# Kernel optimization log

Measured on AMD Instinct MI355X. Metric: run time of the kernel, lower is better.

The kernel has to match this reference:

```python
import jax, jax.numpy as jnp
import numpy as np

EPS = 1e-12

def _safe_norm(x, axis):
    return jnp.sqrt(jnp.sum(x * x, axis=axis) + EPS)

def _forward(z, pos, edge_index, batch, batch_size, emb, centers, gamma,
             fw1, fb1, fw2, fb2, uw1, ub1, uw2, ub2,
             ew1, eb1, ew2, eb2, dipole_w, nac_w,
             aw1, ab1, aw2, ab2, yw1, yb1, yw2, yb2):
    row, col = edge_index[0], edge_index[1]
    N = pos.shape[0]
    diff = pos[col] - pos[row]                    # (E,3)
    dist = _safe_norm(diff, axis=1)               # (E,)
    dirs = diff / (dist[:, None] + 1e-8)          # (E,3)
    rbf = jnp.exp(-gamma * (dist[:, None] - centers) ** 2)   # (E,R)
    s = emb[z]                                    # (N,F)
    v = jnp.zeros((N, s.shape[1], 3), s.dtype)    # (N,F,3)
    n_layers = fw1.shape[0]
    for l in range(n_layers):
        # filter MLP on RBF features -> 3 gates per edge
        phi = jax.nn.silu(rbf @ fw1[l] + fb1[l]) @ fw2[l] + fb2[l]   # (E,3F)
        phi_ss, phi_vv, phi_sv = jnp.split(phi, 3, axis=-1)
        sc = s[col]                                                    # gather (E,F)
        m_s = jax.ops.segment_sum(phi_ss * sc, row, num_segments=N)    # (N,F)
        m_v_e = (phi_vv[..., None] * v[col]
                 + phi_sv[..., None] * dirs[:, None, :] * sc[..., None])  # (E,F,3)
        m_v = jax.ops.segment_sum(m_v_e, row, num_segments=N)          # (N,F,3)
        v_norm = _safe_norm(m_v, axis=-1)                              # (N,F)
        upd = (jax.nn.silu(jnp.concatenate([s, m_s, v_norm], axis=-1) @ uw1[l] + ub1[l])
               @ uw2[l] + ub2[l])                                       # (N,3F)
        delta_s, alpha, beta = jnp.split(upd, 3, axis=-1)
        s = s + delta_s
        v = alpha[..., None] * v + beta[..., None] * m_v
    # energy heads (stacked over states S)
    h = jax.nn.silu(jnp.einsum('nf,sfg->nsg', s, ew1) + eb1)           # (N,S,F)
    e_atom = (jnp.einsum('nsg,sgo->nso', h, ew2) + eb2)[..., 0]        # (N,S)
    energies = jax.ops.segment_sum(e_atom, batch, num_segments=batch_size)  # (M,S)
    dipoles = jax.ops.segment_sum(jnp.einsum('nfk,f->nk', v, dipole_w), batch,
                                  num_segments=batch_size)             # (M,3)
    nac = jax.ops.segment_sum(jnp.einsum('nfk,pf->npk', v, nac_w), batch,
                              num_segments=batch_size)                 # (M,P,3)
    gaps = energies[:, 1:] - energies[:, :1]                           # (M,S-1)
    lam = jax.nn.silu(gaps @ aw1 + ab1) @ aw2 + ab2                    # (M,1)
    nac_mag = _safe_norm(nac, axis=-1)                                 # (M,P)
    phi_y = jax.nn.sigmoid(
        jax.nn.silu(jnp.concatenate([gaps, nac_mag], axis=1) @ yw1 + yb1) @ yw2 + yb2)  # (M,1)
    return energies, dipoles, nac, lam, phi_y

N, E, F, R, L, S, M, A = 20000, 320000, 128, 20, 3, 4, 1000, 100
P = S - 1

def setup_inputs() -> dict:
    key = jax.random.key(0)
    ks = jax.random.split(key, 32)
    w = lambda i, shape, sc=0.05: jax.random.normal(ks[i], shape, jnp.float32) * sc
    return {
        'z': jax.random.randint(ks[0], (N,), 0, A),
        'pos': jax.random.normal(ks[1], (N, 3), jnp.float32),
        'edge_index': jax.random.randint(ks[2], (2, E), 0, N),
        'batch': jnp.sort(jax.random.randint(ks[3], (N,), 0, M)),
        'batch_size': M,
        'emb': jax.random.normal(ks[4], (A, F), jnp.float32),
        'centers': jnp.linspace(0.0, 5.0, R),
        'gamma': jnp.ones((R,), jnp.float32),
        'fw1': w(5, (L, R, F)), 'fb1': jnp.zeros((L, F)),
        'fw2': w(6, (L, F, 3 * F)), 'fb2': jnp.zeros((L, 3 * F)),
        'uw1': w(7, (L, 3 * F, F)), 'ub1': jnp.zeros((L, F)),
        'uw2': w(8, (L, F, 3 * F)), 'ub2': jnp.zeros((L, 3 * F)),
        'ew1': w(9, (S, F, F)), 'eb1': jnp.zeros((S, F)),
        'ew2': w(10, (S, F, 1)), 'eb2': jnp.zeros((S, 1)),
        'dipole_w': jax.random.normal(ks[11], (F,), jnp.float32),
        'nac_w': jax.random.normal(ks[12], (P, F), jnp.float32),
        'aw1': w(13, (S - 1, 64)), 'ab1': jnp.zeros((64,)),
        'aw2': w(14, (64, 1)), 'ab2': jnp.zeros((1,)),
        'yw1': w(15, (S - 1 + P, 128)), 'yb1': jnp.zeros((128,)),
        'yw2': w(16, (128, 1)), 'yb2': jnp.zeros((1,)),
    }

def reference(z, pos, edge_index, batch, batch_size, emb, centers, gamma,
              fw1, fb1, fw2, fb2, uw1, ub1, uw2, ub2,
              ew1, eb1, ew2, eb2, dipole_w, nac_w,
              aw1, ab1, aw2, ab2, yw1, yb1, yw2, yb2):
    return _forward(z, pos, edge_index, batch, batch_size, emb, centers, gamma,
                    fw1, fb1, fw2, fb2, uw1, ub1, uw2, ub2,
                    ew1, eb1, ew2, eb2, dipole_w, nac_w,
                    aw1, ab1, aw2, ab2, yw1, yb1, yw2, yb2)
```

## Files before the change

### kernel.cpp

```cpp
#include <hip/hip_runtime.h>
#include <hip/hip_fp16.h>

#define FDIM 128
#define RDIM 20

#define TAB_T 2048
#define TAB_RANGE 12.0f

constexpr int TH = 256;

__device__ __forceinline__ float siluf(float x) { return x / (1.f + __expf(-x)); }

__device__ __forceinline__ void store_h4(__half* p, float a, float b, float c, float d) {
    __half h[4] = {__float2half(a), __float2half(b), __float2half(c), __float2half(d)};
    *(uint2*)p = *(uint2*)h;
}

typedef _Float16 h2v __attribute__((ext_vector_type(2)));
__device__ __forceinline__ float fdot2u(unsigned int a, unsigned int b, float c) {
    union { unsigned int u; h2v h; } ua, ub;
    ua.u = a; ub.u = b;
    return __builtin_amdgcn_fdot2(ua.h, ub.h, c, false);
}

__global__ void k_init(const int* __restrict__ z, const float* __restrict__ emb,
                       float* __restrict__ s, __half* __restrict__ s_h, int N) {
    int i = blockIdx.x * blockDim.x + threadIdx.x;
    if (i >= N * FDIM) return;
    int n = i >> 7, f = i & 127;
    float val = emb[z[n] * FDIM + f];
    s[i] = val;
    s_h[i] = __float2half(val);
}

__global__ void k_packl(const float* __restrict__ src, unsigned int* __restrict__ dst,
                        int C, int total, size_t sstride, size_t dstride) {
    int l = blockIdx.y;
    const float* sp = src + (size_t)l * sstride;
    unsigned int* dp = dst + (size_t)l * dstride;
    int i = blockIdx.x * 256 + threadIdx.x;
    if (i >= total) return;
    int kp = i / C, c = i - kp * C;
    __half2 h = __halves2half2(__float2half(sp[(2*kp) * C + c]),
                               __float2half(sp[(2*kp+1) * C + c]));
    dp[i] = *(unsigned int*)&h;
}

__global__ void k_hist(const int* __restrict__ erow, int* __restrict__ cursor, int E) {
    int e = blockIdx.x * blockDim.x + threadIdx.x;
    if (e < E) atomicAdd(&cursor[erow[e]], 1);
}

__global__ __launch_bounds__(256) void k_scan1(const int* __restrict__ cursor,
                                               int* __restrict__ rowstart,
                                               int* __restrict__ bsum, int N) {
    __shared__ int sh[256];
    int tid = threadIdx.x;
    int idx = blockIdx.x * 256 + tid;
    int x = (idx < N) ? cursor[idx] : 0;
    sh[tid] = x;
    __syncthreads();
    #pragma unroll
    for (int off = 1; off < 256; off <<= 1) {
        int t = (tid >= off) ? sh[tid - off] : 0;
        __syncthreads();
        sh[tid] += t;
        __syncthreads();
    }
    if (idx < N) rowstart[idx] = sh[tid] - x;
    if (tid == 255) bsum[blockIdx.x] = sh[255];
}

__global__ __launch_bounds__(256) void k_scan2(int* __restrict__ bsum,
                                               int* __restrict__ rowstart, int nb, int N) {
    __shared__ int sh[256];
    __shared__ int carry;
    int tid = threadIdx.x;
    if (tid == 0) carry = 0;
    __syncthreads();
    for (int base = 0; base < nb; base += 256) {
        int idx = base + tid;
        int x = (idx < nb) ? bsum[idx] : 0;
        sh[tid] = x;
        __syncthreads();
        #pragma unroll
        for (int off = 1; off < 256; off <<= 1) {
            int t = (tid >= off) ? sh[tid - off] : 0;
            __syncthreads();
            sh[tid] += t;
            __syncthreads();
        }
        if (idx < nb) bsum[idx] = carry + sh[tid] - x;
        __syncthreads();
        if (tid == 0) carry += sh[255];
        __syncthreads();
    }
    if (tid == 0) rowstart[N] = carry;
}

__global__ __launch_bounds__(256) void k_scan3(int* __restrict__ rowstart,
                                               int* __restrict__ cursor,
                                               const int* __restrict__ bsum, int N) {
    int idx = blockIdx.x * 256 + threadIdx.x;
    if (idx < N) {
        int val = rowstart[idx] + bsum[blockIdx.x];
        rowstart[idx] = val;
        cursor[idx] = val;
    }
}

__global__ void k_fill(const int* __restrict__ erow, int* __restrict__ cursor,
                       int* __restrict__ esort, int E) {
    int e = blockIdx.x * blockDim.x + threadIdx.x;
    if (e < E) {
        int p = atomicAdd(&cursor[erow[e]], 1);
        esort[p] = e;
    }
}

__global__ void k_geom(const float* __restrict__ pos, const int* __restrict__ erow,
                       const int* __restrict__ ecol, const int* __restrict__ esort,
                       int2* __restrict__ geo_ci, float4* __restrict__ geo_wd,
                       float inv_step, int E) {
    int i = blockIdx.x * blockDim.x + threadIdx.x;
    if (i >= E) return;
    int e  = esort[i];
    int rw = erow[e], cl = ecol[e];
    float dx = pos[cl*3+0] - pos[rw*3+0];
    float dy = pos[cl*3+1] - pos[rw*3+1];
    float dz = pos[cl*3+2] - pos[rw*3+2];
    float dist = sqrtf(dx*dx + dy*dy + dz*dz + 1e-12f);
    float inv = 1.f / (dist + 1e-8f);
    float u = fminf(dist * inv_step, (float)TAB_T);
    int t0 = min((int)u, TAB_T - 1);
    geo_ci[i] = make_int2(cl, t0);
    geo_wd[i] = make_float4(u - (float)t0, dx*inv, dy*inv, dz*inv);
}

__global__ __launch_bounds__(TH) void k_table(
    const float* __restrict__ centers, const float* __restrict__ gamma,
    const float* __restrict__ fw1b, const float* __restrict__ fb1b,
    const float* __restrict__ fw2b, const float* __restrict__ fb2b,
    __half* __restrict__ tabb, float step)
{
    __shared__ float sh_rbf[32][RDIM];
    __shared__ float sh_ht[FDIM][33];
    __shared__ float sh_w[32][3 * FDIM + 4];

    const int l   = blockIdx.y;
    const float* fw1 = fw1b + (size_t)l * RDIM * FDIM;
    const float* fb1 = fb1b + (size_t)l * FDIM;
    const float* fw2 = fw2b + (size_t)l * FDIM * 3 * FDIM;
    const float* fb2 = fb2b + (size_t)l * 3 * FDIM;
    __half* tab = tabb + (size_t)l * (TAB_T + 1) * 384;

    const int p0  = blockIdx.x * 32;
    const int tid = threadIdx.x;

    for (int i = tid; i < 32 * RDIM; i += TH) {
        int p = i / RDIM, r = i - p * RDIM;
        float d = (float)(p0 + p) * step - centers[r];
        sh_rbf[p][r] = __expf(-gamma[r] * d * d);
    }
    __syncthreads();
    for (int i = tid; i < 32 * FDIM; i += TH) {
        int p = i >> 7, f = i & 127;
        float acc = fb1[f];
        #pragma unroll
        for (int r = 0; r < RDIM; ++r) acc += sh_rbf[p][r] * fw1[r * FDIM + f];
        sh_ht[f][p] = siluf(acc);
    }

    const int eq = tid & 7;
    const int fq = tid >> 3;
    const int f0 = fq * 4;

    float pg[3][4][4];
    #pragma unroll
    for (int g3 = 0; g3 < 3; ++g3)
        #pragma unroll
        for (int ee = 0; ee < 4; ++ee)
            #pragma unroll
            for (int i = 0; i < 4; ++i) pg[g3][ee][i] = fb2[g3 * FDIM + f0 + i];

    const int kkr = tid >> 3;
    const int t8  = tid & 7;
    for (int kc = 0; kc < 4; ++kc) {
        __syncthreads();
        #pragma unroll
        for (int j = 0; j < 12; ++j) {
            int g = (t8 * 12 + j) * 4;
            float4 w4 = *(const float4*)&fw2[(size_t)(kc * 32 + kkr) * (3 * FDIM) + g];
            *(float4*)&sh_w[kkr][g] = w4;
        }
        __syncthreads();
        #pragma unroll 4
        for (int kk = 0; kk < 32; ++kk) {
            float hv[4];
            #pragma unroll
            for (int ee = 0; ee < 4; ++ee) hv[ee] = sh_ht[kc * 32 + kk][4 * eq + ee];
            #pragma unroll
            for (int g3 = 0; g3 < 3; ++g3) {
                float4 w4 = *(const float4*)&sh_w[kk][g3 * FDIM + f0];
                #pragma unroll
                for (int ee = 0; ee < 4; ++ee) {
                    pg[g3][ee][0] += hv[ee] * w4.x;
                    pg[g3][ee][1] += hv[ee] * w4.y;
                    pg[g3][ee][2] += hv[ee] * w4.z;
                    pg[g3][ee][3] += hv[ee] * w4.w;
                }
            }
        }
    }

    #pragma unroll
    for (int ee = 0; ee < 4; ++ee) {
        int pt = p0 + 4 * eq + ee;
        if (pt <= TAB_T) {
            #pragma unroll
            for (int g3 = 0; g3 < 3; ++g3)
                store_h4(&tab[(size_t)pt * 384 + g3 * FDIM + f0],
                         pg[g3][ee][0], pg[g3][ee][1], pg[g3][ee][2], pg[g3][ee][3]);
        }
    }
}

__global__ __launch_bounds__(256) void k_repack(const __half* __restrict__ tab,
                                                __half2* __restrict__ tab2) {
    int l = blockIdx.y;
    const __half* t  = tab  + (size_t)l * (TAB_T + 1) * 384;
    __half2*      t2 = tab2 + (size_t)l * TAB_T * 384;
    int i = blockIdx.x * 256 + threadIdx.x;
    t2[i] = __halves2half2(t[i], t[i + 384]);
}

__global__ __launch_bounds__(128) void k_gather(
    const int* __restrict__ rowstart,
    const int2* __restrict__ geo_ci, const float4* __restrict__ geo_wd,
    const __half2* __restrict__ tab2, const __half* __restrict__ s_h,
    const __half* __restrict__ v_h,
    __half* __restrict__ m_s_h, __half* __restrict__ vnorm_h, __half* __restrict__ m_v_h,
    int withv, int N)
{
    __shared__ int   sh_col[32];
    __shared__ int   sh_t0[32];
    __shared__ float sh_w[32];
    __shared__ float sh_d0[32], sh_d1[32], sh_d2[32];

    const int n   = blockIdx.x;
    const int tid = threadIdx.x;
    const int lo  = rowstart[n], hi = rowstart[n + 1];

    float acc_s = 0.f, av0 = 0.f, av1 = 0.f, av2 = 0.f;

    for (int base = lo; base < hi; base += 32) {
        const int ne = min(32, hi - base);
        __syncthreads();
        if (tid < 32) {
            int idx = base + tid;
            if (tid < ne) {
                int2   ci = geo_ci[idx];
                float4 wd = geo_wd[idx];
                sh_col[tid] = ci.x; sh_t0[tid] = ci.y;
                sh_w[tid] = wd.x;
                sh_d0[tid] = wd.y; sh_d1[tid] = wd.z; sh_d2[tid] = wd.w;
            } else {
                sh_col[tid] = 0; sh_t0[tid] = 0; sh_w[tid] = 0.f;
                sh_d0[tid] = sh_d1[tid] = sh_d2[tid] = 0.f;
            }
        }
        __syncthreads();
        if (withv) {
            #pragma unroll 2
            for (int el = 0; el < ne; ++el) {
                int   cl = sh_col[el];
                int   t0 = sh_t0[el];
                float w  = sh_w[el];
                const __half2* t2 = tab2 + (size_t)t0 * 384 + tid;
                float2 pss2 = __half22float2(t2[0]);
                float2 pvv2 = __half22float2(t2[128]);
                float2 psv2 = __half22float2(t2[256]);
                float pss = pss2.x + w * (pss2.y - pss2.x);
                float pvv = pvv2.x + w * (pvv2.y - pvv2.x);
                float psv = psv2.x + w * (psv2.y - psv2.x);
                float sc = __half2float(s_h[(size_t)cl * FDIM + tid]);
                const __half* vp = v_h + (size_t)cl * 3 * FDIM + tid;
                float svs = psv * sc;
                acc_s += pss * sc;
                av0 += pvv * __half2float(vp[0])        + svs * sh_d0[el];
                av1 += pvv * __half2float(vp[FDIM])     + svs * sh_d1[el];
                av2 += pvv * __half2float(vp[2*FDIM])   + svs * sh_d2[el];
            }
        } else {
            #pragma unroll 2
            for (int el = 0; el < ne; ++el) {
                int   cl = sh_col[el];
                int   t0 = sh_t0[el];
                float w  = sh_w[el];
                const __half2* t2 = tab2 + (size_t)t0 * 384 + tid;
                float2 pss2 = __half22float2(t2[0]);
                float2 psv2 = __half22float2(t2[256]);
                float pss = pss2.x + w * (pss2.y - pss2.x);
                float psv = psv2.x + w * (psv2.y - psv2.x);
                float sc = __half2float(s_h[(size_t)cl * FDIM + tid]);
                float svs = psv * sc;
                acc_s += pss * sc;
                av0 += svs * sh_d0[el];
                av1 += svs * sh_d1[el];
                av2 += svs * sh_d2[el];
            }
        }
    }

    m_s_h[(size_t)n * FDIM + tid]  = __float2half(acc_s);
    vnorm_h[(size_t)n * FDIM + tid] = __float2half(sqrtf(av0*av0 + av1*av1 + av2*av2 + 1e-12f));
    __half* mh = m_v_h + (size_t)n * 3 * FDIM + tid;
    mh[0]      = __float2half(av0);
    mh[FDIM]   = __float2half(av1);
    mh[2*FDIM] = __float2half(av2);
}

__global__ __launch_bounds__(128) void k_mlp1(
    const __half* __restrict__ s_h, const __half* __restrict__ m_s_h,
    const __half* __restrict__ vnorm_h,
    const unsigned int* __restrict__ uw1p,
    const float* __restrict__ ub1,
    __half* __restrict__ u1_h, int N)
{
    __shared__ unsigned int shA2[8][36];
    __shared__ unsigned int shB2[8][68];

    const int tid = threadIdx.x;
    const int n0  = blockIdx.x * 32;
    const int cb  = blockIdx.y * 64;
    const int tx  = tid & 15, ty = tid >> 4;
    const int cA  = tx * 4;
    const int r0  = ty * 4;
    const int rs  = tid >> 2;
    const int kp0 = (tid & 3) * 2;

    float acc[4][4];
    {
        float4 b4 = *(const float4*)&ub1[cb + cA];
        #pragma unroll
        for (int i = 0; i < 4; ++i) {
            acc[i][0] = b4.x; acc[i][1] = b4.y; acc[i][2] = b4.z; acc[i][3] = b4.w;
        }
    }

    uint2 pa; uint4 pb;

#define MLP1_LOAD(kc) do { \
        pa = make_uint2(0u, 0u); \
        { int kg = (kc) * 16 + (tid & 3) * 4; int n = n0 + rs; \
          if (n < N) { \
              const __half* base; \
              if (kg < 128)      base = &s_h[(size_t)n * FDIM + kg]; \
              else if (kg < 256) base = &m_s_h[(size_t)n * FDIM + kg - 128]; \
              else               base = &vnorm_h[(size_t)n * FDIM + kg - 256]; \
              pa = *(const uint2*)base; } } \
        pb = *(const uint4*)&uw1p[(size_t)((kc)*8 + ty) * FDIM + cb + 4*tx]; \
    } while (0)

    MLP1_LOAD(0);
    for (int kc = 0; kc < 24; ++kc) {
        __syncthreads();
        shA2[kp0][rs]     = pa.x;
        shA2[kp0 + 1][rs] = pa.y;
        *(uint4*)&shB2[ty][4*tx] = pb;
        if (kc + 1 < 24) MLP1_LOAD(kc + 1);
        __syncthreads();
        #pragma unroll
        for (int kp = 0; kp < 8; ++kp) {
            unsigned int b0 = shB2[kp][cA+0], b1 = shB2[kp][cA+1];
            unsigned int b2 = shB2[kp][cA+2], b3 = shB2[kp][cA+3];
            #pragma unroll
            for (int i = 0; i < 4; ++i) {
                unsigned int ai = shA2[kp][r0 + i];
                acc[i][0] = fdot2u(ai, b0, acc[i][0]);
                acc[i][1] = fdot2u(ai, b1, acc[i][1]);
                acc[i][2] = fdot2u(ai, b2, acc[i][2]);
                acc[i][3] = fdot2u(ai, b3, acc[i][3]);
            }
        }
    }
#undef MLP1_LOAD

    #pragma unroll
    for (int i = 0; i < 4; ++i) {
        int n = n0 + r0 + i;
        if (n < N) {
            store_h4(&u1_h[(size_t)n * FDIM + cb + cA],
                     siluf(acc[i][0]), siluf(acc[i][1]), siluf(acc[i][2]), siluf(acc[i][3]));
        }
    }
}

__global__ __launch_bounds__(128) void k_mlp2(
    const __half* __restrict__ u1_h,
    const unsigned int* __restrict__ uw2p,
    const float* __restrict__ ub2,
    float* __restrict__ s, __half* __restrict__ v_h, const __half* __restrict__ m_v_h,
    __half* __restrict__ s_h, int N)
{
    __shared__ unsigned int shU2[64][33];
    __shared__ unsigned int shB2[8][68];

    const int tid = threadIdx.x;
    const int n0  = blockIdx.x * 32;
    const int cb  = blockIdx.y * 64;
    const int tx  = tid & 15, ty = tid >> 4;
    const int cA  = tx * 4;
    const int r0  = ty * 4;

    #pragma unroll
    for (int it = 0; it < 4; ++it) {
        int idx = it * 128 + tid;
        int row = idx >> 4;
        int c8  = (idx & 15) * 8;
        int n = n0 + row;
        uint4 u = make_uint4(0u,0u,0u,0u);
        if (n < N) u = *(const uint4*)&u1_h[(size_t)n * FDIM + c8];
        int kpb = c8 >> 1;
        shU2[kpb + 0][row] = u.x;
        shU2[kpb + 1][row] = u.y;
        shU2[kpb + 2][row] = u.z;
        shU2[kpb + 3][row] = u.w;
    }

    uint4 pb;
#define MLP2_LOADB(g, kc) do { \
        pb = *(const uint4*)&uw2p[(size_t)((kc)*8 + ty) * (3*FDIM) + (g) * FDIM + cb + 4*tx]; \
    } while (0)

    MLP2_LOADB(0, 0);
    float alpha[4][4];

    for (int g = 0; g < 3; ++g) {
        float acc2[4][4];
        {
            float4 b4 = *(const float4*)&ub2[g * FDIM + cb + cA];
            #pragma unroll
            for (int i = 0; i < 4; ++i) {
                acc2[i][0]=b4.x; acc2[i][1]=b4.y; acc2[i][2]=b4.z; acc2[i][3]=b4.w;
            }
        }
        for (int kc = 0; kc < 8; ++kc) {
            __syncthreads();
            *(uint4*)&shB2[ty][4*tx] = pb;
            if (kc + 1 < 8)      MLP2_LOADB(g, kc + 1);
            else if (g + 1 < 3)  MLP2_LOADB(g + 1, 0);
            __syncthreads();
            #pragma unroll
            for (int kp = 0; kp < 8; ++kp) {
                int kpg = kc * 8 + kp;
                unsigned int b0 = shB2[kp][cA+0], b1 = shB2[kp][cA+1];
                unsigned int b2 = shB2[kp][cA+2], b3 = shB2[kp][cA+3];
                #pragma unroll
                for (int i = 0; i < 4; ++i) {
                    unsigned int uv = shU2[kpg][r0 + i];
                    acc2[i][0] = fdot2u(uv, b0, acc2[i][0]);
                    acc2[i][1] = fdot2u(uv, b1, acc2[i][1]);
                    acc2[i][2] = fdot2u(uv, b2, acc2[i][2]);
                    acc2[i][3] = fdot2u(uv, b3, acc2[i][3]);
                }
            }
        }

        if (g == 0) {
            #pragma unroll
            for (int i = 0; i < 4; ++i) {
                int n = n0 + r0 + i;
                if (n < N) {
                    float4 s0 = *(const float4*)&s[(size_t)n * FDIM + cb + cA];
                    s0.x += acc2[i][0]; s0.y += acc2[i][1]; s0.z += acc2[i][2]; s0.w += acc2[i][3];
                    *(float4*)&s[(size_t)n * FDIM + cb + cA] = s0;
                    store_h4(&s_h[(size_t)n * FDIM + cb + cA], s0.x, s0.y, s0.z, s0.w);
                }
            }
        } else if (g == 1) {
            #pragma unroll
            for (int i = 0; i < 4; ++i)
                #pragma unroll
                for (int j = 0; j < 4; ++j) alpha[i][j] = acc2[i][j];
        } else {
            #pragma unroll
            for (int i = 0; i < 4; ++i) {
                int n = n0 + r0 + i;
                if (n < N) {
                    #pragma unroll
                    for (int k = 0; k < 3; ++k) {
                        __half* vhp = v_h + ((size_t)n * 3 + k) * FDIM + cb + cA;
                        const __half* mp = m_v_h + ((size_t)n * 3 + k) * FDIM + cb + cA;
                        __half vh[4], mh[4];
                        *(uint2*)vh = *(const uint2*)vhp;
                        *(uint2*)mh = *(const uint2*)mp;
                        float nv[4];
                        #pragma unroll
                        for (int j = 0; j < 4; ++j)
                            nv[j] = alpha[i][j] * __half2float(vh[j])
                                  + acc2[i][j] * __half2float(mh[j]);
                        store_h4(vhp, nv[0], nv[1], nv[2], nv[3]);
                    }
                }
            }
        }
    }
#undef MLP2_LOADB
}

__global__ __launch_bounds__(256) void k_energy3(
    const unsigned int* __restrict__ ew1p,
    const float* __restrict__ eb1,
    const float* __restrict__ ew2, const float* __restrict__ eb2,
    const __half* __restrict__ s_h, const int* __restrict__ batch,
    float* __restrict__ energies, int N, int S)
{
    __shared__ unsigned int shA2[64][66];
    __shared__ unsigned int shB2[8][132];

    const int tid = threadIdx.x;
    const int n0  = blockIdx.x * 64;
    const int st  = blockIdx.y;
    const int tx  = tid & 15, ty = tid >> 4;
    const int cA  = tx * 4, cB = 64 + tx * 4;
    const int r0  = ty * 4;

    #pragma unroll
    for (int it = 0; it < 4; ++it) {
        int idx = it * 256 + tid;
        int row = idx >> 4;
        int c8  = (idx & 15) * 8;
        int n = n0 + row;
        uint4 u = make_uint4(0u,0u,0u,0u);
        if (n < N) u = *(const uint4*)&s_h[(size_t)n * FDIM + c8];
        int kpb = c8 >> 1;
        shA2[kpb + 0][row] = u.x;
        shA2[kpb + 1][row] = u.y;
        shA2[kpb + 2][row] = u.z;
        shA2[kpb + 3][row] = u.w;
    }

    uint2 pb;
#define EN_LOADB(kc) do { \
        pb = *(const uint2*)&ew1p[(size_t)st * 64 * FDIM + (size_t)((kc)*8 + (tid >> 6)) * FDIM + 2*(tid & 63)]; \
    } while (0)

    EN_LOADB(0);
    float acc[4][8];
    {
        float4 bA = *(const float4*)&eb1[st * FDIM + cA];
        float4 bB = *(const float4*)&eb1[st * FDIM + cB];
        #pragma unroll
        for (int i = 0; i < 4; ++i) {
            acc[i][0]=bA.x; acc[i][1]=bA.y; acc[i][2]=bA.z; acc[i][3]=bA.w;
            acc[i][4]=bB.x; acc[i][5]=bB.y; acc[i][6]=bB.z; acc[i][7]=bB.w;
        }
    }

    uint2 pb2;
#define EN_LOADB2(kc) do { \
        pb2 = *(const uint2*)&ew1p[(size_t)st * 64 * FDIM + (size_t)((kc)*8 + 4 + (tid >> 6)) * FDIM + 2*(tid & 63)]; \
    } while (0)

    EN_LOADB2(0);
    for (int kc = 0; kc < 8; ++kc) {
        __syncthreads();
        {
            int kp = tid >> 6;
            int c2 = 2 * (tid & 63);
            shB2[kp][c2]     = pb.x;  shB2[kp][c2 + 1]     = pb.y;
            shB2[kp + 4][c2] = pb2.x; shB2[kp + 4][c2 + 1] = pb2.y;
        }
        if (kc + 1 < 8) { EN_LOADB(kc + 1); EN_LOADB2(kc + 1); }
        __syncthreads();
        #pragma unroll
        for (int kp = 0; kp < 8; ++kp) {
            int kpg = kc * 8 + kp;
            unsigned int b0 = shB2[kp][cA+0], b1 = shB2[kp][cA+1];
            unsigned int b2 = shB2[kp][cA+2], b3 = shB2[kp][cA+3];
            unsigned int b4 = shB2[kp][cB+0], b5 = shB2[kp][cB+1];
            unsigned int b6 = shB2[kp][cB+2], b7 = shB2[kp][cB+3];
            #pragma unroll
            for (int i = 0; i < 4; ++i) {
                unsigned int ai = shA2[kpg][r0 + i];
                acc[i][0] = fdot2u(ai, b0, acc[i][0]);
                acc[i][1] = fdot2u(ai, b1, acc[i][1]);
                acc[i][2] = fdot2u(ai, b2, acc[i][2]);
                acc[i][3] = fdot2u(ai, b3, acc[i][3]);
                acc[i][4] = fdot2u(ai, b4, acc[i][4]);
                acc[i][5] = fdot2u(ai, b5, acc[i][5]);
                acc[i][6] = fdot2u(ai, b6, acc[i][6]);
                acc[i][7] = fdot2u(ai, b7, acc[i][7]);
            }
        }
    }
#undef EN_LOADB
#undef EN_LOADB2

    float4 wA = *(const float4*)&ew2[st * FDIM + cA];
    float4 wB = *(const float4*)&ew2[st * FDIM + cB];
    float p[4];
    #pragma unroll
    for (int i = 0; i < 4; ++i) {
        p[i]  = siluf(acc[i][0])*wA.x + siluf(acc[i][1])*wA.y
              + siluf(acc[i][2])*wA.z + siluf(acc[i][3])*wA.w;
        p[i] += siluf(acc[i][4])*wB.x + siluf(acc[i][5])*wB.y
              + siluf(acc[i][6])*wB.z + siluf(acc[i][7])*wB.w;
    }
    #pragma unroll
    for (int m = 1; m <= 8; m <<= 1) {
        #pragma unroll
        for (int i = 0; i < 4; ++i) p[i] += __shfl_xor(p[i], m, 64);
    }
    if (tx == 0) {
        float b2 = eb2[st];
        #pragma unroll
        for (int i = 0; i < 4; ++i) {
            int n = n0 + r0 + i;
            if (n < N) atomicAdd(&energies[batch[n] * S + st], p[i] + b2);
        }
    }
}

__global__ void k_vec(const __half* __restrict__ v_h, const float* __restrict__ dipole_w,
                      const float* __restrict__ nac_w, const int* __restrict__ batch,
                      float* __restrict__ dipoles, float* __restrict__ nac, int N)
{
    int n = blockIdx.x * 4 + (threadIdx.x >> 6);
    int lane = threadIdx.x & 63;
    if (n >= N) return;
    float pd[3] = {0.f, 0.f, 0.f};
    float pn[3][3] = {{0.f}};
    const __half* vb = v_h + (size_t)n * 3 * FDIM;
    for (int f = lane; f < FDIM; f += 64) {
        float v0 = __half2float(vb[f]);
        float v1 = __half2float(vb[FDIM + f]);
        float v2 = __half2float(vb[2*FDIM + f]);
        float wd = dipole_w[f];
        pd[0] += wd * v0; pd[1] += wd * v1; pd[2] += wd * v2;
        #pragma unroll
        for (int p = 0; p < 3; ++p) {
            float wn = nac_w[p * FDIM + f];
            pn[p][0] += wn * v0; pn[p][1] += wn * v1; pn[p][2] += wn * v2;
        }
    }
    #pragma unroll
    for (int d = 32; d > 0; d >>= 1) {
        #pragma unroll
        for (int k = 0; k < 3; ++k) pd[k] += __shfl_down(pd[k], d, 64);
        #pragma unroll
        for (int p = 0; p < 3; ++p)
            #pragma unroll
            for (int k = 0; k < 3; ++k) pn[p][k] += __shfl_down(pn[p][k], d, 64);
    }
    if (lane == 0) {
        int m = batch[n];
        #pragma unroll
        for (int k = 0; k < 3; ++k) atomicAdd(&dipoles[m * 3 + k], pd[k]);
        #pragma unroll
        for (int p = 0; p < 3; ++p)
            #pragma unroll
            for (int k = 0; k < 3; ++k) atomicAdd(&nac[(m * 3 + p) * 3 + k], pn[p][k]);
    }
}

__global__ __launch_bounds__(128) void k_heads(
    const float* __restrict__ aw1, const float* __restrict__ ab1,
    const float* __restrict__ aw2, const float* __restrict__ ab2,
    const float* __restrict__ yw1, const float* __restrict__ yb1,
    const float* __restrict__ yw2, const float* __restrict__ yb2,
    const float* __restrict__ energies, const float* __restrict__ nac,
    float* __restrict__ lam, float* __restrict__ phi_y, int M, int S)
{
    __shared__ float sh_in[8];
    __shared__ float sh_red[2];
    int m = blockIdx.x;
    if (m >= M) return;
    int tid = threadIdx.x;
    if (tid == 0) {
        float e0 = energies[m * S];
        for (int j = 0; j < 3; ++j) sh_in[j] = energies[m * S + 1 + j] - e0;
        for (int p = 0; p < 3; ++p) {
            float a = nac[(m * 3 + p) * 3 + 0];
            float b = nac[(m * 3 + p) * 3 + 1];
            float c = nac[(m * 3 + p) * 3 + 2];
            sh_in[3 + p] = sqrtf(a*a + b*b + c*c + 1e-12f);
        }
    }
    __syncthreads();
    float pa = 0.f;
    if (tid < 64) {
        float h = ab1[tid];
        #pragma unroll
        for (int j = 0; j < 3; ++j) h += sh_in[j] * aw1[j * 64 + tid];
        pa = siluf(h) * aw2[tid];
    }
    float h2 = yb1[tid];
    #pragma unroll
    for (int j = 0; j < 6; ++j) h2 += sh_in[j] * yw1[j * 128 + tid];
    float py = siluf(h2) * yw2[tid];
    #pragma unroll
    for (int d = 32; d > 0; d >>= 1) {
        pa += __shfl_down(pa, d, 64);
        py += __shfl_down(py, d, 64);
    }
    int wid = tid >> 6, lane = tid & 63;
    if (lane == 0) sh_red[wid] = py;
    __syncthreads();
    if (tid == 0) {
        lam[m] = pa + ab2[0];
        float yt = sh_red[0] + sh_red[1] + yb2[0];
        phi_y[m] = 1.f / (1.f + __expf(-yt));
    }
}

extern "C" void kernel_launch(void* const* d_in, const int* in_sizes, int n_in,
                              void* d_out, int out_size, void* d_ws, size_t ws_size,
                              hipStream_t stream)
{
    const int*   z        = (const int*)  d_in[0];
    const float* pos      = (const float*)d_in[1];
    const int*   eidx     = (const int*)  d_in[2];
    const int*   batch    = (const int*)  d_in[3];
    const float* emb      = (const float*)d_in[5];
    const float* centers  = (const float*)d_in[6];
    const float* gamma    = (const float*)d_in[7];
    const float* fw1      = (const float*)d_in[8];
    const float* fb1      = (const float*)d_in[9];
    const float* fw2      = (const float*)d_in[10];
    const float* fb2      = (const float*)d_in[11];
    const float* uw1      = (const float*)d_in[12];
    const float* ub1      = (const float*)d_in[13];
    const float* uw2      = (const float*)d_in[14];
    const float* ub2      = (const float*)d_in[15];
    const float* ew1      = (const float*)d_in[16];
    const float* eb1      = (const float*)d_in[17];
    const float* ew2      = (const float*)d_in[18];
    const float* eb2      = (const float*)d_in[19];
    const float* dipole_w = (const float*)d_in[20];
    const float* nac_w    = (const float*)d_in[21];
    const float* aw1      = (const float*)d_in[22];
    const float* ab1      = (const float*)d_in[23];
    const float* aw2      = (const float*)d_in[24];
    const float* ab2      = (const float*)d_in[25];
    const float* yw1      = (const float*)d_in[26];
    const float* yb1      = (const float*)d_in[27];
    const float* yw2      = (const float*)d_in[28];
    const float* yb2      = (const float*)d_in[29];

    const int N = in_sizes[0];
    const int E = in_sizes[2] / 2;
    const int S = in_sizes[19];
    const int P = in_sizes[21] / FDIM;
    const int L = in_sizes[9] / FDIM;
    const int M = out_size / (S + 3 + P * 3 + 2);

    const size_t NF = (size_t)N * FDIM;
    float*   s       = (float*)d_ws;
    __half*  s_h     = (__half*)(s + NF);
    __half*  v_h     = s_h + NF;
    __half*  m_s_h   = v_h + 3 * NF;
    __half*  vnorm_h = m_s_h + NF;
    __half*  m_v_h   = vnorm_h + NF;
    __half*  u1_hb   = m_v_h + 3 * NF;
    unsigned int* uw1p = (unsigned int*)(u1_hb + NF);
    unsigned int* uw2p = uw1p + (size_t)L * 192 * 128;
    unsigned int* ew1p = uw2p + (size_t)L * 64 * 384;
    __half*  tab     = (__half*)(ew1p + (size_t)S * 64 * 128);
    __half2* tab2    = (__half2*)(tab + (size_t)L * (TAB_T + 1) * 384);
    float4*  geo_wd  = (float4*)(tab2 + (size_t)L * TAB_T * 384);
    int2*    geo_ci  = (int2*)(geo_wd + E);
    int* rowstart = (int*)(geo_ci + E);
    int* cursor   = rowstart + (N + 1);
    int* esort    = cursor + N;
    int* bsum     = esort + E;

    float* out      = (float*)d_out;
    float* energies = out;
    float* dipoles  = energies + (size_t)M * S;
    float* nac      = dipoles  + (size_t)M * 3;
    float* lam      = nac      + (size_t)M * P * 3;
    float* phi_y    = lam      + M;

    const int* erow = eidx;
    const int* ecol = eidx + E;

    const float step = TAB_RANGE / (float)TAB_T;
    const float inv_step = (float)TAB_T / TAB_RANGE;
    const int NB  = (N + 63) / 64;
    const int NB2 = (N + 31) / 32;
    const int NSB = (N + 255) / 256;

    hipMemsetAsync(d_out, 0, (size_t)out_size * sizeof(float), stream);
    hipMemsetAsync(cursor, 0, (size_t)N * sizeof(int), stream);
    hipMemsetAsync(v_h, 0, 3 * NF * sizeof(__half), stream);
    k_hist<<<(E + 255) / 256, 256, 0, stream>>>(erow, cursor, E);
    k_scan1<<<NSB, 256, 0, stream>>>(cursor, rowstart, bsum, N);
    k_scan2<<<1, 256, 0, stream>>>(bsum, rowstart, NSB, N);
    k_scan3<<<NSB, 256, 0, stream>>>(rowstart, cursor, bsum, N);
    k_fill<<<(E + 255) / 256, 256, 0, stream>>>(erow, cursor, esort, E);
    k_geom<<<(E + 255) / 256, 256, 0, stream>>>(pos, erow, ecol, esort, geo_ci, geo_wd, inv_step, E);
    k_init<<<(N * FDIM + 255) / 256, 256, 0, stream>>>(z, emb, s, s_h, N);

    k_packl<<<dim3((192*128 + 255) / 256, L), 256, 0, stream>>>(
        uw1, uw1p, 128, 192 * 128, (size_t)3 * FDIM * FDIM, (size_t)192 * 128);
    k_packl<<<dim3((64*384 + 255) / 256, L), 256, 0, stream>>>(
        uw2, uw2p, 384, 64 * 384, (size_t)FDIM * 3 * FDIM, (size_t)64 * 384);
    k_packl<<<dim3((64*128 + 255) / 256, S), 256, 0, stream>>>(
        ew1, ew1p, 128, 64 * 128, (size_t)FDIM * FDIM, (size_t)64 * 128);

    const int tab_blocks = (TAB_T + 1 + 31) / 32;
    k_table<<<dim3(tab_blocks, L), TH, 0, stream>>>(centers, gamma, fw1, fb1, fw2, fb2, tab, step);
    k_repack<<<dim3(TAB_T * 384 / 256, L), 256, 0, stream>>>(tab, tab2);

    for (int l = 0; l < L; ++l) {
        const __half2* tab2_l = tab2 + (size_t)l * TAB_T * 384;
        k_gather<<<N, 128, 0, stream>>>(
            rowstart, geo_ci, geo_wd, tab2_l, s_h, v_h,
            m_s_h, vnorm_h, m_v_h, (l > 0) ? 1 : 0, N);
        k_mlp1<<<dim3(NB2, 2), 128, 0, stream>>>(
            s_h, m_s_h, vnorm_h,
            uw1p + (size_t)l * 192 * 128, ub1 + (size_t)l * FDIM, u1_hb, N);
        k_mlp2<<<dim3(NB2, 2), 128, 0, stream>>>(
            u1_hb, uw2p + (size_t)l * 64 * 384, ub2 + (size_t)l * 3 * FDIM,
            s, v_h, m_v_h, s_h, N);
    }

    k_energy3<<<dim3(NB, S), 256, 0, stream>>>(ew1p, eb1, ew2, eb2, s_h, batch, energies, N, S);
    k_vec<<<(N + 3) / 4, 256, 0, stream>>>(v_h, dipole_w, nac_w, batch, dipoles, nac, N);
    k_heads<<<M, 128, 0, stream>>>(aw1, ab1, aw2, ab2, yw1, yb1, yw2, yb2,
                                   energies, nac, lam, phi_y, M, S);
}
```

Before: 505.5 us.

## Fuse edge fill with geometry, interleave filter table into uint4, vectorise head loads

Merges the CSR fill and geometry kernels, so each edge atomically claims its slot and writes its geometry record there directly, which removes the esort array and one launch. The filter table is repacked so that the three gate pairs for each table point and feature sit in one 16-byte uint4, letting the gather kernel fetch them with a single load instead of three strided half2 loads. This costs about a third more table memory because of the padding word. The energy kernel now issues both B-tile loads in one macro, and the vector-head kernel replaces its strided loop with half2 and float2 vector loads; both are small cleanups.

```diff
diff --git a/kernel.cpp b/kernel.cpp
--- a/kernel.cpp
+++ b/kernel.cpp
@@ -21,6 +21,10 @@
     union { unsigned int u; h2v h; } ua, ub;
     ua.u = a; ub.u = b;
     return __builtin_amdgcn_fdot2(ua.h, ub.h, c, false);
+}
+
+__device__ __forceinline__ float2 h2f2(unsigned int u) {
+    return __half22float2(*(const __half2*)&u);
 }
 
 __global__ void k_init(const int* __restrict__ z, const float* __restrict__ emb,
@@ -109,23 +113,14 @@
     }
 }
 
-__global__ void k_fill(const int* __restrict__ erow, int* __restrict__ cursor,
-                       int* __restrict__ esort, int E) {
+__global__ void k_fillgeo(const float* __restrict__ pos, const int* __restrict__ erow,
+                          const int* __restrict__ ecol, int* __restrict__ cursor,
+                          int2* __restrict__ geo_ci, float4* __restrict__ geo_wd,
+                          float inv_step, int E) {
     int e = blockIdx.x * blockDim.x + threadIdx.x;
-    if (e < E) {
-        int p = atomicAdd(&cursor[erow[e]], 1);
-        esort[p] = e;
-    }
-}
-
-__global__ void k_geom(const float* __restrict__ pos, const int* __restrict__ erow,
-                       const int* __restrict__ ecol, const int* __restrict__ esort,
-                       int2* __restrict__ geo_ci, float4* __restrict__ geo_wd,
-                       float inv_step, int E) {
-    int i = blockIdx.x * blockDim.x + threadIdx.x;
-    if (i >= E) return;
-    int e  = esort[i];
+    if (e >= E) return;
     int rw = erow[e], cl = ecol[e];
+    int p = atomicAdd(&cursor[rw], 1);
     float dx = pos[cl*3+0] - pos[rw*3+0];
     float dy = pos[cl*3+1] - pos[rw*3+1];
     float dz = pos[cl*3+2] - pos[rw*3+2];
@@ -133,8 +128,8 @@
     float inv = 1.f / (dist + 1e-8f);
     float u = fminf(dist * inv_step, (float)TAB_T);
     int t0 = min((int)u, TAB_T - 1);
-    geo_ci[i] = make_int2(cl, t0);
-    geo_wd[i] = make_float4(u - (float)t0, dx*inv, dy*inv, dz*inv);
+    geo_ci[p] = make_int2(cl, t0);
+    geo_wd[p] = make_float4(u - (float)t0, dx*inv, dy*inv, dz*inv);
 }
 
 __global__ __launch_bounds__(TH) void k_table(
@@ -225,19 +220,29 @@
     }
 }
 
-__global__ __launch_bounds__(256) void k_repack(const __half* __restrict__ tab,
-                                                __half2* __restrict__ tab2) {
+__global__ __launch_bounds__(256) void k_repack4(const __half* __restrict__ tab,
+                                                 uint4* __restrict__ tab4) {
     int l = blockIdx.y;
-    const __half* t  = tab  + (size_t)l * (TAB_T + 1) * 384;
-    __half2*      t2 = tab2 + (size_t)l * TAB_T * 384;
+    const __half* t = tab + (size_t)l * (TAB_T + 1) * 384;
+    uint4* t4 = tab4 + (size_t)l * TAB_T * 128;
     int i = blockIdx.x * 256 + threadIdx.x;
-    t2[i] = __halves2half2(t[i], t[i + 384]);
+    int tt = i >> 7, f = i & 127;
+    const __half* tp = t + (size_t)tt * 384;
+    __half2 ss = __halves2half2(tp[f],       tp[384 + f]);
+    __half2 vv = __halves2half2(tp[128 + f], tp[512 + f]);
+    __half2 sv = __halves2half2(tp[256 + f], tp[640 + f]);
+    uint4 o;
+    o.x = *(unsigned int*)&ss;
+    o.y = *(unsigned int*)&vv;
+    o.z = *(unsigned int*)&sv;
+    o.w = 0u;
+    t4[i] = o;
 }
 
 __global__ __launch_bounds__(128) void k_gather(
     const int* __restrict__ rowstart,
     const int2* __restrict__ geo_ci, const float4* __restrict__ geo_wd,
-    const __half2* __restrict__ tab2, const __half* __restrict__ s_h,
+    const uint4* __restrict__ tab4, const __half* __restrict__ s_h,
     const __half* __restrict__ v_h,
     __half* __restrict__ m_s_h, __half* __restrict__ vnorm_h, __half* __restrict__ m_v_h,
     int withv, int N)
@@ -276,10 +281,10 @@
                 int   cl = sh_col[el];
                 int   t0 = sh_t0[el];
                 float w  = sh_w[el];
-                const __half2* t2 = tab2 + (size_t)t0 * 384 + tid;
-                float2 pss2 = __half22float2(t2[0]);
-                float2 pvv2 = __half22float2(t2[128]);
-                float2 psv2 = __half22float2(t2[256]);
+                uint4 tv = tab4[(size_t)t0 * 128 + tid];
+                float2 pss2 = h2f2(tv.x);
+                float2 pvv2 = h2f2(tv.y);
+                float2 psv2 = h2f2(tv.z);
                 float pss = pss2.x + w * (pss2.y - pss2.x);
                 float pvv = pvv2.x + w * (pvv2.y - pvv2.x);
                 float psv = psv2.x + w * (psv2.y - psv2.x);
@@ -297,9 +302,9 @@
                 int   cl = sh_col[el];
                 int   t0 = sh_t0[el];
                 float w  = sh_w[el];
-                const __half2* t2 = tab2 + (size_t)t0 * 384 + tid;
-                float2 pss2 = __half22float2(t2[0]);
-                float2 psv2 = __half22float2(t2[256]);
+                uint4 tv = tab4[(size_t)t0 * 128 + tid];
+                float2 pss2 = h2f2(tv.x);
+                float2 psv2 = h2f2(tv.z);
                 float pss = pss2.x + w * (pss2.y - pss2.x);
                 float psv = psv2.x + w * (psv2.y - psv2.x);
                 float sc = __half2float(s_h[(size_t)cl * FDIM + tid]);
@@ -541,9 +546,10 @@
         shA2[kpb + 3][row] = u.w;
     }
 
-    uint2 pb;
+    uint2 pb, pb2;
 #define EN_LOADB(kc) do { \
         pb = *(const uint2*)&ew1p[(size_t)st * 64 * FDIM + (size_t)((kc)*8 + (tid >> 6)) * FDIM + 2*(tid & 63)]; \
+        pb2 = *(const uint2*)&ew1p[(size_t)st * 64 * FDIM + (size_t)((kc)*8 + 4 + (tid >> 6)) * FDIM + 2*(tid & 63)]; \
     } while (0)
 
     EN_LOADB(0);
@@ -558,12 +564,6 @@
         }
     }
 
-    uint2 pb2;
-#define EN_LOADB2(kc) do { \
-        pb2 = *(const uint2*)&ew1p[(size_t)st * 64 * FDIM + (size_t)((kc)*8 + 4 + (tid >> 6)) * FDIM + 2*(tid & 63)]; \
-    } while (0)
-
-    EN_LOADB2(0);
     for (int kc = 0; kc < 8; ++kc) {
         __syncthreads();
         {
@@ -572,7 +572,7 @@
             shB2[kp][c2]     = pb.x;  shB2[kp][c2 + 1]     = pb.y;
             shB2[kp + 4][c2] = pb2.x; shB2[kp + 4][c2 + 1] = pb2.y;
         }
-        if (kc + 1 < 8) { EN_LOADB(kc + 1); EN_LOADB2(kc + 1); }
+        if (kc + 1 < 8) EN_LOADB(kc + 1);
         __syncthreads();
         #pragma unroll
         for (int kp = 0; kp < 8; ++kp) {
@@ -596,7 +596,6 @@
         }
     }
 #undef EN_LOADB
-#undef EN_LOADB2
 
     float4 wA = *(const float4*)&ew2[st * FDIM + cA];
     float4 wB = *(const float4*)&ew2[st * FDIM + cB];
@@ -630,20 +629,23 @@
     int n = blockIdx.x * 4 + (threadIdx.x >> 6);
     int lane = threadIdx.x & 63;
     if (n >= N) return;
-    float pd[3] = {0.f, 0.f, 0.f};
-    float pn[3][3] = {{0.f}};
+    int f2 = lane * 2;
     const __half* vb = v_h + (size_t)n * 3 * FDIM;
-    for (int f = lane; f < FDIM; f += 64) {
-        float v0 = __half2float(vb[f]);
-        float v1 = __half2float(vb[FDIM + f]);
-        float v2 = __half2float(vb[2*FDIM + f]);
-        float wd = dipole_w[f];
-        pd[0] += wd * v0; pd[1] += wd * v1; pd[2] += wd * v2;
-        #pragma unroll
-        for (int p = 0; p < 3; ++p) {
-            float wn = nac_w[p * FDIM + f];
-            pn[p][0] += wn * v0; pn[p][1] += wn * v1; pn[p][2] += wn * v2;
-        }
+    float2 v0 = __half22float2(*(const __half2*)&vb[f2]);
+    float2 v1 = __half22float2(*(const __half2*)&vb[FDIM + f2]);
+    float2 v2 = __half22float2(*(const __half2*)&vb[2*FDIM + f2]);
+    float2 wd = *(const float2*)&dipole_w[f2];
+    float pd[3];
+    pd[0] = wd.x * v0.x + wd.y * v0.y;
+    pd[1] = wd.x * v1.x + wd.y * v1.y;
+    pd[2] = wd.x * v2.x + wd.y * v2.y;
+    float pn[3][3];
+    #pragma unroll
+    for (int p = 0; p < 3; ++p) {
+        float2 wn = *(const float2*)&nac_w[p * FDIM + f2];
+        pn[p][0] = wn.x * v0.x + wn.y * v0.y;
+        pn[p][1] = wn.x * v1.x + wn.y * v1.y;
+        pn[p][2] = wn.x * v2.x + wn.y * v2.y;
     }
     #pragma unroll
     for (int d = 32; d > 0; d >>= 1) {
@@ -768,13 +770,12 @@
     unsigned int* uw2p = uw1p + (size_t)L * 192 * 128;
     unsigned int* ew1p = uw2p + (size_t)L * 64 * 384;
     __half*  tab     = (__half*)(ew1p + (size_t)S * 64 * 128);
-    __half2* tab2    = (__half2*)(tab + (size_t)L * (TAB_T + 1) * 384);
-    float4*  geo_wd  = (float4*)(tab2 + (size_t)L * TAB_T * 384);
+    uint4*   tab4    = (uint4*)(tab + (size_t)L * (TAB_T + 1) * 384);
+    float4*  geo_wd  = (float4*)(tab4 + (size_t)L * TAB_T * 128);
     int2*    geo_ci  = (int2*)(geo_wd + E);
     int* rowstart = (int*)(geo_ci + E);
     int* cursor   = rowstart + (N + 1);
-    int* esort    = cursor + N;
-    int* bsum     = esort + E;
+    int* bsum     = cursor + N;
 
     float* out      = (float*)d_out;
     float* energies = out;
@@ -799,8 +800,8 @@
     k_scan1<<<NSB, 256, 0, stream>>>(cursor, rowstart, bsum, N);
     k_scan2<<<1, 256, 0, stream>>>(bsum, rowstart, NSB, N);
     k_scan3<<<NSB, 256, 0, stream>>>(rowstart, cursor, bsum, N);
-    k_fill<<<(E + 255) / 256, 256, 0, stream>>>(erow, cursor, esort, E);
-    k_geom<<<(E + 255) / 256, 256, 0, stream>>>(pos, erow, ecol, esort, geo_ci, geo_wd, inv_step, E);
+    k_fillgeo<<<(E + 255) / 256, 256, 0, stream>>>(pos, erow, ecol, cursor,
+                                                   geo_ci, geo_wd, inv_step, E);
     k_init<<<(N * FDIM + 255) / 256, 256, 0, stream>>>(z, emb, s, s_h, N);
 
     k_packl<<<dim3((192*128 + 255) / 256, L), 256, 0, stream>>>(
@@ -812,12 +813,12 @@
 
     const int tab_blocks = (TAB_T + 1 + 31) / 32;
     k_table<<<dim3(tab_blocks, L), TH, 0, stream>>>(centers, gamma, fw1, fb1, fw2, fb2, tab, step);
-    k_repack<<<dim3(TAB_T * 384 / 256, L), 256, 0, stream>>>(tab, tab2);
+    k_repack4<<<dim3(TAB_T * 128 / 256, L), 256, 0, stream>>>(tab, tab4);
 
     for (int l = 0; l < L; ++l) {
-        const __half2* tab2_l = tab2 + (size_t)l * TAB_T * 384;
+        const uint4* tab4_l = tab4 + (size_t)l * TAB_T * 128;
         k_gather<<<N, 128, 0, stream>>>(
-            rowstart, geo_ci, geo_wd, tab2_l, s_h, v_h,
+            rowstart, geo_ci, geo_wd, tab4_l, s_h, v_h,
             m_s_h, vnorm_h, m_v_h, (l > 0) ? 1 : 0, N);
         k_mlp1<<<dim3(NB2, 2), 128, 0, stream>>>(
             s_h, m_s_h, vnorm_h,
```

Measured after the change: 550.9 us. 9.0% more time.
